# Performance work log

Hardware: AMD Instinct MI355X
Metric: run time of the kernel (lower is better)

Reference implementation:

```python
import jax, jax.numpy as jnp
import numpy as np

IN_F = 256
OUT_F = 256
H = 4
DH = OUT_F // H  # 64
N = 6144


def setup_inputs() -> dict:
    key = jax.random.key(0)
    ks = jax.random.split(key, 6)
    x = jax.random.normal(ks[0], (N, IN_F), dtype=jnp.float32)
    adj = jax.random.randint(ks[1], (N, N), 0, 2, dtype=jnp.int32)
    # per-head Linear(in_features, d_head): weights [H, IN_F, DH], bias [H, DH]
    W = jax.random.normal(ks[2], (H, IN_F, DH), dtype=jnp.float32) / np.sqrt(IN_F)
    Wb = jax.random.normal(ks[3], (H, DH), dtype=jnp.float32) * 0.01
    # per-head Linear(2*d_head, 1): weights [H, 2*DH], bias [H]
    A = jax.random.normal(ks[4], (H, 2 * DH), dtype=jnp.float32) / np.sqrt(2 * DH)
    Ab = jax.random.normal(ks[5], (H,), dtype=jnp.float32) * 0.01
    return {"x": x, "adj": adj, "W": W, "Wb": Wb, "A": A, "Ab": Ab}


def reference(x, adj, W, Wb, A, Ab):
    # h[h,n,d] = per-head linear projection of node features
    h = jnp.einsum("ni,hid->hnd", x, W) + Wb[:, None, :]
    a_src, a_dst = A[:, :DH], A[:, DH:]
    # score(i,j) = a_src . h_i + a_dst . h_j + b  (decomposed concat-linear)
    s_src = jnp.einsum("hnd,hd->hn", h, a_src) + Ab[:, None]  # [H, N]
    s_dst = jnp.einsum("hnd,hd->hn", h, a_dst)                # [H, N]
    scores = s_src[:, :, None] + s_dst[:, None, :]            # [H, N, N]
    # Faithful to source: non-edges get score 0.0 (not -inf) before softmax
    scores = jnp.where(adj[None, :, :] > 0, scores, 0.0)
    probs = jax.nn.softmax(scores, axis=-1)                   # row softmax
    out = jnp.einsum("hij,hjd->hid", probs, h)                # [H, N, DH]
    # concat heads along feature dim -> [N, H*DH]
    return jnp.transpose(out, (1, 0, 2)).reshape(N, H * DH)
```

## Files before the change

kernel.cpp:

```cpp
#include <hip/hip_runtime.h>
#include <stdint.h>

#define NN 6144
#define NC 576

typedef float f32x4 __attribute__((ext_vector_type(4)));
typedef __bf16 bf16x8v __attribute__((ext_vector_type(8)));

__device__ __forceinline__ unsigned short f2bf(float f) {
  unsigned u = __float_as_uint(f);
  u += 0x7FFFu + ((u >> 16) & 1u);
  return (unsigned short)(u >> 16);
}

__device__ __forceinline__ float bf2f(unsigned short s) {
  unsigned u = (unsigned)s << 16;
  return __uint_as_float(u);
}

__device__ __forceinline__ unsigned char f2e4m3(float f) {
  unsigned u = __float_as_uint(f);
  unsigned sgn = (u >> 24) & 0x80u;
  unsigned au = u & 0x7FFFFFFFu;
  if (au >= 0x43E00000u) return (unsigned char)(sgn | 0x7E);
  if (au < 0x3C800000u) {
    int q = (int)rintf(__uint_as_float(au) * 512.0f);
    return (unsigned char)(sgn | (q >= 8 ? 0x08 : q));
  }
  unsigned r = au + 0x7FFFFu + ((au >> 20) & 1u);
  int e = (int)(r >> 23) - 127;
  unsigned m = (r >> 20) & 7u;
  return (unsigned char)(sgn | ((unsigned)(e + 7) << 3) | m);
}

__device__ __forceinline__ unsigned short pack2(float a, float b) {
  return (unsigned short)f2e4m3(a) | ((unsigned short)f2e4m3(b) << 8);
}

__device__ __forceinline__ void async_load16(const void* g, void* l) {
  __builtin_amdgcn_global_load_lds(
      (__attribute__((address_space(1))) void*)(uintptr_t)g,
      (__attribute__((address_space(3))) void*)(uint32_t)(uintptr_t)l,
      16, 0, 0);
}

__global__ __launch_bounds__(256) void p0s(
    const float* __restrict__ W,
    const float* __restrict__ Aw, const float* __restrict__ Wb,
    unsigned short* __restrict__ wsw, float* __restrict__ Acat,
    float* __restrict__ T)
{
  const int bid = blockIdx.x, t = threadIdx.x;
  if (bid < 8) {
#pragma unroll
    for (int i = 0; i < 4; ++i) {
      const int e = bid * 256 + t + i * 2048;
      const int l = e & 63, kc = (e >> 6) & 7, ct = e >> 9;
      const int c = ct * 16 + (l & 15);
      const int h = c >> 6, d0 = c & 63;
      const int ks = kc * 32 + (l >> 4) * 8;
      const float* src = W + h * 16384 + ks * 64 + d0;
      unsigned uu[4];
#pragma unroll
      for (int j = 0; j < 4; ++j)
        uu[j] = (unsigned)f2bf(src[(2*j) * 64]) | ((unsigned)f2bf(src[(2*j+1) * 64]) << 16);
      *(uint4*)(wsw + (size_t)e * 8) = (uint4){uu[0], uu[1], uu[2], uu[3]};
    }
    return;
  }
  T[t] = 0.f;
  const int h = t >> 6, d = t & 63;
  Acat[t]       = Aw[h * 128 + d];
  Acat[256 + t] = Aw[h * 128 + 64 + d];
  Acat[512 + t] = Wb[t];
}

__global__ __launch_bounds__(256) void k1m(
    const float* __restrict__ x, const unsigned short* __restrict__ wsw,
    const float* __restrict__ Acat, const float* __restrict__ Ab,
    const int* __restrict__ adj, unsigned* __restrict__ bm,
    unsigned char* __restrict__ V8, float* __restrict__ e_src, float* __restrict__ T)
{
  __shared__ unsigned char lsh[16384];
  __shared__ float lt[256];
  const int t = threadIdx.x;

  if (blockIdx.x >= 192) {
    const int pb = blockIdx.x - 192;
    const int tid = pb * 256 + t;
    const int4* src = (const int4*)adj + (size_t)tid * 8;
    int4 q[8];
#pragma unroll
    for (int j = 0; j < 8; ++j) q[j] = src[j];
    unsigned b = 0;
#pragma unroll
    for (int j = 0; j < 8; ++j) {
      unsigned nib = (unsigned)q[j].x | ((unsigned)q[j].y << 1) |
                     ((unsigned)q[j].z << 2) | ((unsigned)q[j].w << 3);
      b |= nib << (4 * j);
    }
    bm[tid] = b;
    return;
  }

  const int w = t >> 6, l = t & 63;
  const int v = blockIdx.x * 4 + w;
  const int mt = v >> 1, nh = v & 1;
  const int i0 = mt * 16, c0 = nh * 128;
  const int lm = l & 15, lk = l >> 4;

  {
    unsigned short* lx = (unsigned short*)lsh;
    const float* xb = x + (size_t)(blockIdx.x * 32) * 256;
#pragma unroll
    for (int j = 0; j < 4; ++j) {
      const int e = t + j * 256;
      const int tile = e >> 9, e9 = e & 511;
      const int el = e9 & 63, kc = e9 >> 6;
      const int node = tile * 16 + (el & 15);
      const int ks = kc * 32 + (el >> 4) * 8;
      const float4* xp = (const float4*)(xb + (size_t)node * 256 + ks);
      float4 v0 = xp[0], v1 = xp[1];
      uint4 o;
      o.x = (unsigned)f2bf(v0.x) | ((unsigned)f2bf(v0.y) << 16);
      o.y = (unsigned)f2bf(v0.z) | ((unsigned)f2bf(v0.w) << 16);
      o.z = (unsigned)f2bf(v1.x) | ((unsigned)f2bf(v1.y) << 16);
      o.w = (unsigned)f2bf(v1.z) | ((unsigned)f2bf(v1.w) << 16);
      *(uint4*)(lx + (size_t)e * 8) = o;
    }
  }
  lt[t] = 0.f;
  __syncthreads();

  f32x4 acc[8];
#pragma unroll
  for (int nt = 0; nt < 8; ++nt) acc[nt] = (f32x4){0.f, 0.f, 0.f, 0.f};

  const unsigned short* ap = (const unsigned short*)lsh + (((size_t)(w >> 1)) * 512 + l) * 8;
  const unsigned short* bp = wsw + ((size_t)nh * 4096 + l) * 8;

#pragma unroll
  for (int kc = 0; kc < 8; ++kc) {
    bf16x8v a = *(const bf16x8v*)(ap + (size_t)kc * 512);
#pragma unroll
    for (int nt = 0; nt < 8; ++nt) {
      bf16x8v b = *(const bf16x8v*)(bp + ((size_t)nt * 512 + kc * 64) * 8);
      acc[nt] = __builtin_amdgcn_mfma_f32_16x16x32_bf16(a, b, acc[nt], 0, 0, 0);
    }
  }

  float asv[8], adv[8];
#pragma unroll
  for (int nt = 0; nt < 8; ++nt) {
    const int cc = c0 + nt * 16 + lm;
    const float wb = Acat[512 + cc];
#pragma unroll
    for (int rr = 0; rr < 4; ++rr) acc[nt][rr] += wb;
    asv[nt] = Acat[cc];
    adv[nt] = Acat[256 + cc];
  }

#pragma unroll
  for (int nt = 0; nt < 8; ++nt)
    atomicAdd(&lt[c0 + nt * 16 + lm], acc[nt][0] + acc[nt][1] + acc[nt][2] + acc[nt][3]);

  float ss[2][4], sd[2][4];
#pragma unroll
  for (int hl = 0; hl < 2; ++hl)
#pragma unroll
    for (int rr = 0; rr < 4; ++rr) {
      float s1 = 0.f, s2 = 0.f;
#pragma unroll
      for (int j = 0; j < 4; ++j) {
        s1 += acc[hl * 4 + j][rr] * asv[hl * 4 + j];
        s2 += acc[hl * 4 + j][rr] * adv[hl * 4 + j];
      }
      ss[hl][rr] = s1; sd[hl][rr] = s2;
    }
#pragma unroll
  for (int off = 1; off < 16; off <<= 1)
#pragma unroll
    for (int hl = 0; hl < 2; ++hl)
#pragma unroll
      for (int rr = 0; rr < 4; ++rr) {
        ss[hl][rr] += __shfl_xor(ss[hl][rr], off);
        sd[hl][rr] += __shfl_xor(sd[hl][rr], off);
      }

  float ed[2][4];
#pragma unroll
  for (int hl = 0; hl < 2; ++hl)
#pragma unroll
    for (int rr = 0; rr < 4; ++rr) ed[hl][rr] = expf(sd[hl][rr]);

  if (lm == 0) {
#pragma unroll
    for (int hl = 0; hl < 2; ++hl) {
      const int hh = nh * 2 + hl;
      const float ab = Ab[hh];
#pragma unroll
      for (int rr = 0; rr < 4; ++rr)
        e_src[(size_t)hh * NN + i0 + lk * 4 + rr] = expf(ss[hl][rr] + ab);
    }
  }

  __syncthreads();

  unsigned char* mylv = lsh + w * 4096;
#pragma unroll
  for (int nt = 0; nt < 8; ++nt) {
    const int hl = nt >> 2;
    const int d = (nt & 3) * 16 + lm;
    const int lcE = hl * 128 + d;
    const int lcP = lcE + 64;
    *(unsigned short*)(mylv + lcE * 16 + lk * 4)     = pack2(ed[hl][0] * acc[nt][0], ed[hl][1] * acc[nt][1]);
    *(unsigned short*)(mylv + lcE * 16 + lk * 4 + 2) = pack2(ed[hl][2] * acc[nt][2], ed[hl][3] * acc[nt][3]);
    *(unsigned short*)(mylv + lcP * 16 + lk * 4)     = pack2(acc[nt][0], acc[nt][1]);
    *(unsigned short*)(mylv + lcP * 16 + lk * 4 + 2) = pack2(acc[nt][2], acc[nt][3]);
  }
#pragma unroll
  for (int j = 0; j < 4; ++j) {
    const int lc = j * 64 + l;
    uint4 val = *(const uint4*)(mylv + lc * 16);
    *(uint4*)(V8 + (size_t)(nh * 256 + lc) * NN + i0) = val;
  }
  if (lm == 0) {
#pragma unroll
    for (int hl = 0; hl < 2; ++hl) {
      const int hh = nh * 2 + hl;
      unsigned char* pq = V8 + (size_t)(512 + hh) * NN + i0 + lk * 4;
      *(unsigned short*)pq       = pack2(ed[hl][0], ed[hl][1]);
      *(unsigned short*)(pq + 2) = pack2(ed[hl][2], ed[hl][3]);
    }
    if (nh == 0)
      *(unsigned*)(V8 + (size_t)516 * NN + i0 + lk * 4) = 0x38383838u;
  }

  __syncthreads();
  atomicAdd(&T[t], lt[t]);
}

__global__ __launch_bounds__(256, 3) void k2_gemm(
    const unsigned* __restrict__ bm, const unsigned char* __restrict__ V8,
    unsigned short* __restrict__ out2b, float* __restrict__ out2e, int nks)
{
  __shared__ unsigned char lB[2][144 * 128];
  const int t   = threadIdx.x;
  const int ks  = blockIdx.x / 192;
  const int r   = blockIdx.x - ks * 192;
  const int cb  = r & 3;
  const int rb  = r >> 2;
  const int krange = NN / nks;
  const int i0 = rb * 128, n0 = cb * 144, k0 = ks * krange;
  const int w = t >> 6, l = t & 63;
  const int lm = l & 15, lk = l >> 4;

  f32x4 acc[2][9];
#pragma unroll
  for (int mt = 0; mt < 2; ++mt)
#pragma unroll
    for (int nt = 0; nt < 9; ++nt) acc[mt][nt] = (f32x4){0.f, 0.f, 0.f, 0.f};

  int scol[5], sgr[5];
#pragma unroll
  for (int u = 0; u < 5; ++u) {
    const int gi = u * 256 + t;
    scol[u] = gi >> 3;
    sgr[u]  = (gi & 7) ^ (scol[u] & 7);
  }
  const int dbase4 = (1024 + (t & ~63)) * 16;

  const unsigned* gA0 = bm + (size_t)(i0 + w * 32 + lm) * (NN / 32) + (k0 >> 5) + lk;
  const unsigned char* gBb = V8 + (size_t)n0 * NN + k0;

  const int iters = krange / 128;

#define K2_STAGE(BUF, IT)                                                        \
  do {                                                                           \
    const unsigned char* gB = gBb + (IT) * 128;                                  \
    _Pragma("unroll")                                                            \
    for (int u = 0; u < 4; ++u)                                                  \
      async_load16(gB + (size_t)scol[u] * NN + sgr[u] * 16,                      \
                   (char*)lB[BUF] + (size_t)(u * 256 + (t & ~63)) * 16);         \
    if (t < 128)                                                                 \
      async_load16(gB + (size_t)scol[4] * NN + sgr[4] * 16,                      \
                   (char*)lB[BUF] + dbase4);                                     \
  } while (0)

  unsigned bits_c[2], bits_n[2];
  K2_STAGE(0, 0);
#pragma unroll
  for (int mt = 0; mt < 2; ++mt) bits_c[mt] = gA0[(size_t)mt * 16 * (NN / 32)];
  __syncthreads();

  int cur = 0;
  for (int it = 0; it < iters; ++it) {
    if (it + 1 < iters) {
      K2_STAGE(cur ^ 1, it + 1);
#pragma unroll
      for (int mt = 0; mt < 2; ++mt)
        bits_n[mt] = gA0[(size_t)mt * 16 * (NN / 32) + (it + 1) * 4];
    }

    longlong2 afr[2][2];
#pragma unroll
    for (int mt = 0; mt < 2; ++mt) {
      unsigned u[8];
#pragma unroll
      for (int i = 0; i < 8; ++i) {
        unsigned nib = (bits_c[mt] >> (4 * i)) & 0xFu;
        u[i] = ((nib * 0x00204081u) & 0x01010101u) << 3;
      }
      afr[mt][0].x = (long long)(((unsigned long long)u[1] << 32) | u[0]);
      afr[mt][0].y = (long long)(((unsigned long long)u[3] << 32) | u[2]);
      afr[mt][1].x = (long long)(((unsigned long long)u[5] << 32) | u[4]);
      afr[mt][1].y = (long long)(((unsigned long long)u[7] << 32) | u[6]);
    }

#pragma unroll
    for (int b = 0; b < 2; ++b) {
#pragma unroll
      for (int nt = 0; nt < 9; ++nt) {
        const int cc = nt * 16 + lm;
        const int pos = (lk * 2 + b) ^ (cc & 7);
        longlong2 bv = *(const longlong2*)(lB[cur] + cc * 128 + pos * 16);
#pragma unroll
        for (int mt = 0; mt < 2; ++mt) {
          acc[mt][nt] = __builtin_amdgcn_mfma_f32_16x16x32_fp8_fp8(
              afr[mt][b].x, bv.x, acc[mt][nt], 0, 0, 0);
          acc[mt][nt] = __builtin_amdgcn_mfma_f32_16x16x32_fp8_fp8(
              afr[mt][b].y, bv.y, acc[mt][nt], 0, 0, 0);
        }
      }
    }

    if (it + 1 < iters) {
#pragma unroll
      for (int mt = 0; mt < 2; ++mt) bits_c[mt] = bits_n[mt];
    }
    __syncthreads();
    cur ^= 1;
  }
#undef K2_STAGE

  unsigned short* lw = (unsigned short*)((char*)lB[0] + w * 4608);
  float* oe = out2e + (size_t)ks * ((size_t)NN * 64);
  unsigned short* pb = out2b + ((size_t)(ks * 4 + cb) * NN + i0 + w * 32) * 144;
#pragma unroll
  for (int mt = 0; mt < 2; ++mt) {
#pragma unroll
    for (int nt = 0; nt < 9; ++nt) {
      const int coll = nt * 16 + lm;
#pragma unroll
      for (int rr = 0; rr < 4; ++rr)
        lw[(lk * 4 + rr) * 144 + coll] = f2bf(acc[mt][nt][rr] * 64.0f);
      if (cb == 3 && nt >= 5) {
        const int row = i0 + w * 32 + mt * 16 + lk * 4;
#pragma unroll
        for (int rr = 0; rr < 4; ++rr)
          oe[(size_t)(row + rr) * 64 + (n0 + coll - 512)] = acc[mt][nt][rr] * 64.0f;
      }
    }
    const uint4* ls = (const uint4*)((char*)lB[0] + w * 4608);
    char* dst = (char*)(pb + (size_t)mt * 16 * 144);
    for (int s = l; s < 288; s += 64)
      *(uint4*)(dst + s * 16) = ls[s];
  }
}

__global__ __launch_bounds__(256) void k3_final(
    const unsigned short* __restrict__ out2b, const float* __restrict__ out2e,
    const float* __restrict__ e_src, const float* __restrict__ T,
    float* __restrict__ out, int nks)
{
  const int n = blockIdx.x, c = threadIdx.x;
  const int h = c >> 6, d = c & 63;
  const int cS = h * 128 + d, cP = cS + 64;
  const int cbS = cS / 144, ofS = cS % 144;
  const int cbP = cP / 144, ofP = cP % 144;
  float Se = 0.f, Sp = 0.f, E = 0.f, dg = 0.f;
  for (int s = 0; s < nks; ++s) {
    const unsigned short* base = out2b + (size_t)s * 4 * NN * 144;
    Se += bf2f(base[((size_t)cbS * NN + n) * 144 + ofS]);
    Sp += bf2f(base[((size_t)cbP * NN + n) * 144 + ofP]);
    const float* re = out2e + (size_t)s * NN * 64 + (size_t)n * 64;
    E  += re[h];
    dg += re[4];
  }
  float e = e_src[h * NN + n];
  float D = e * E + ((float)NN - dg);
  out[(size_t)n * 256 + c] = (e * Se + (T[c] - Sp)) / D;
}

extern "C" void kernel_launch(void* const* d_in, const int* in_sizes, int n_in,
                              void* d_out, int out_size, void* d_ws, size_t ws_size,
                              hipStream_t stream) {
  const float* x  = (const float*)d_in[0];
  const int*   adj= (const int*)d_in[1];
  const float* W  = (const float*)d_in[2];
  const float* Wb = (const float*)d_in[3];
  const float* Aw = (const float*)d_in[4];
  const float* Ab = (const float*)d_in[5];
  float* out = (float*)d_out;
  char* ws = (char*)d_ws;
  unsigned char* V8 = (unsigned char*)ws;
  float* e_src = (float*)(ws + 3538944);
  float* T     = (float*)(ws + 3637248);
  float* Acat  = (float*)(ws + 3638272);
  unsigned short* wsw = (unsigned short*)(ws + 3641344);
  unsigned* bm = (unsigned*)(ws + 6918144);
  unsigned short* out2b = (unsigned short*)(ws + 44666880);
  float* out2e = (float*)(ws + 87134208);

  const size_t slabB = (size_t)4 * NN * 144 * 2;
  const size_t slabE = (size_t)NN * 64 * 4;
  int nks = 2;
  if (ws_size >= 44666880 + 4 * slabB + 4 * slabE)  nks = 4;

  hipLaunchKernelGGL(p0s, dim3(9), dim3(256), 0, stream,
                     W, Aw, Wb, wsw, Acat, T);
  hipLaunchKernelGGL(k1m, dim3(4800), dim3(256), 0, stream,
                     x, wsw, Acat, Ab, adj, bm, V8, e_src, T);
  hipLaunchKernelGGL(k2_gemm, dim3(192 * nks), dim3(256), 0, stream, bm, V8, out2b, out2e, nks);
  hipLaunchKernelGGL(k3_final, dim3(NN), dim3(256), 0, stream, out2b, out2e, e_src, T, out, nks);
}
```

Before: 271.7 us.

## Load GEMM B operand directly from global memory instead of LDS double buffer

```diff
diff --git a/kernel.cpp b/kernel.cpp
--- a/kernel.cpp
+++ b/kernel.cpp
@@ -35,13 +35,6 @@
 
 __device__ __forceinline__ unsigned short pack2(float a, float b) {
   return (unsigned short)f2e4m3(a) | ((unsigned short)f2e4m3(b) << 8);
-}
-
-__device__ __forceinline__ void async_load16(const void* g, void* l) {
-  __builtin_amdgcn_global_load_lds(
-      (__attribute__((address_space(1))) void*)(uintptr_t)g,
-      (__attribute__((address_space(3))) void*)(uint32_t)(uintptr_t)l,
-      16, 0, 0);
 }
 
 __global__ __launch_bounds__(256) void p0s(
@@ -244,7 +237,7 @@
     const unsigned* __restrict__ bm, const unsigned char* __restrict__ V8,
     unsigned short* __restrict__ out2b, float* __restrict__ out2e, int nks)
 {
-  __shared__ unsigned char lB[2][144 * 128];
+  __shared__ unsigned char lE[4][4608];
   const int t   = threadIdx.x;
   const int ks  = blockIdx.x / 192;
   const int r   = blockIdx.x - ks * 192;
@@ -261,46 +254,15 @@
 #pragma unroll
     for (int nt = 0; nt < 9; ++nt) acc[mt][nt] = (f32x4){0.f, 0.f, 0.f, 0.f};
 
-  int scol[5], sgr[5];
-#pragma unroll
-  for (int u = 0; u < 5; ++u) {
-    const int gi = u * 256 + t;
-    scol[u] = gi >> 3;
-    sgr[u]  = (gi & 7) ^ (scol[u] & 7);
-  }
-  const int dbase4 = (1024 + (t & ~63)) * 16;
-
   const unsigned* gA0 = bm + (size_t)(i0 + w * 32 + lm) * (NN / 32) + (k0 >> 5) + lk;
-  const unsigned char* gBb = V8 + (size_t)n0 * NN + k0;
+  const unsigned char* gB0 = V8 + (size_t)(n0 + lm) * NN + k0 + lk * 32;
 
   const int iters = krange / 128;
-
-#define K2_STAGE(BUF, IT)                                                        \
-  do {                                                                           \
-    const unsigned char* gB = gBb + (IT) * 128;                                  \
-    _Pragma("unroll")                                                            \
-    for (int u = 0; u < 4; ++u)                                                  \
-      async_load16(gB + (size_t)scol[u] * NN + sgr[u] * 16,                      \
-                   (char*)lB[BUF] + (size_t)(u * 256 + (t & ~63)) * 16);         \
-    if (t < 128)                                                                 \
-      async_load16(gB + (size_t)scol[4] * NN + sgr[4] * 16,                      \
-                   (char*)lB[BUF] + dbase4);                                     \
-  } while (0)
-
-  unsigned bits_c[2], bits_n[2];
-  K2_STAGE(0, 0);
-#pragma unroll
-  for (int mt = 0; mt < 2; ++mt) bits_c[mt] = gA0[(size_t)mt * 16 * (NN / 32)];
-  __syncthreads();
-
-  int cur = 0;
   for (int it = 0; it < iters; ++it) {
-    if (it + 1 < iters) {
-      K2_STAGE(cur ^ 1, it + 1);
-#pragma unroll
-      for (int mt = 0; mt < 2; ++mt)
-        bits_n[mt] = gA0[(size_t)mt * 16 * (NN / 32) + (it + 1) * 4];
-    }
+    unsigned bits[2];
+#pragma unroll
+    for (int mt = 0; mt < 2; ++mt)
+      bits[mt] = gA0[(size_t)mt * 16 * (NN / 32) + it * 4];
 
     longlong2 afr[2][2];
 #pragma unroll
@@ -308,7 +270,7 @@
       unsigned u[8];
 #pragma unroll
       for (int i = 0; i < 8; ++i) {
-        unsigned nib = (bits_c[mt] >> (4 * i)) & 0xFu;
+        unsigned nib = (bits[mt] >> (4 * i)) & 0xFu;
         u[i] = ((nib * 0x00204081u) & 0x01010101u) << 3;
       }
       afr[mt][0].x = (long long)(((unsigned long long)u[1] << 32) | u[0]);
@@ -317,13 +279,12 @@
       afr[mt][1].y = (long long)(((unsigned long long)u[7] << 32) | u[6]);
     }
 
+    const unsigned char* gBi = gB0 + it * 128;
 #pragma unroll
     for (int b = 0; b < 2; ++b) {
 #pragma unroll
       for (int nt = 0; nt < 9; ++nt) {
-        const int cc = nt * 16 + lm;
-        const int pos = (lk * 2 + b) ^ (cc & 7);
-        longlong2 bv = *(const longlong2*)(lB[cur] + cc * 128 + pos * 16);
+        longlong2 bv = *(const longlong2*)(gBi + (size_t)(nt * 16) * NN + b * 16);
 #pragma unroll
         for (int mt = 0; mt < 2; ++mt) {
           acc[mt][nt] = __builtin_amdgcn_mfma_f32_16x16x32_fp8_fp8(
@@ -333,17 +294,9 @@
         }
       }
     }
-
-    if (it + 1 < iters) {
-#pragma unroll
-      for (int mt = 0; mt < 2; ++mt) bits_c[mt] = bits_n[mt];
-    }
-    __syncthreads();
-    cur ^= 1;
-  }
-#undef K2_STAGE
-
-  unsigned short* lw = (unsigned short*)((char*)lB[0] + w * 4608);
+  }
+
+  unsigned short* lw = (unsigned short*)lE[w];
   float* oe = out2e + (size_t)ks * ((size_t)NN * 64);
   unsigned short* pb = out2b + ((size_t)(ks * 4 + cb) * NN + i0 + w * 32) * 144;
 #pragma unroll
@@ -361,7 +314,7 @@
           oe[(size_t)(row + rr) * 64 + (n0 + coll - 512)] = acc[mt][nt][rr] * 64.0f;
       }
     }
-    const uint4* ls = (const uint4*)((char*)lB[0] + w * 4608);
+    const uint4* ls = (const uint4*)lE[w];
     char* dst = (char*)(pb + (size_t)mt * 16 * 144);
     for (int s = l; s < 288; s += 64)
       *(uint4*)(dst + s * 16) = ls[s];
```

Result: slower. 318.4 us (+17.2%).
